# Kernel tuning notes

Hardware: AMD Instinct MI355X
Metric: run time of the kernel (lower is better)

## Reference

```python
import jax, jax.numpy as jnp
import numpy as np

B, T, V, C, K = 64, 128, 25, 128, 128
R = max(K // 4, 1)


def _ln(x, w, b, eps=1e-5):
    mu = jnp.mean(x, axis=-1, keepdims=True)
    var = jnp.mean((x - mu) ** 2, axis=-1, keepdims=True)
    return (x - mu) * jax.lax.rsqrt(var + eps) * w + b


def setup_inputs() -> dict:
    key = jax.random.key(0)
    ks = jax.random.split(key, 24)
    def w(i, shape, scale=0.05):
        return jax.random.normal(ks[i], shape, dtype=jnp.float32) * scale
    return {
        "x": jax.random.normal(ks[0], (B, T, V, C), dtype=jnp.float32),
        "A": jnp.broadcast_to(jnp.eye(V, dtype=jnp.float32), (K, V, V)) + 0.0,
        "lam": jnp.float32(0.1),
        "phi_w": w(1, (C, K)), "phi_b": w(2, (K,)),
        "theta_w": w(3, (C, K)), "theta_b": w(4, (K,)),
        "kappa_w": w(5, (K, K)), "kappa_b": w(6, (K,)),
        "xi_w": w(7, (C, K)), "xi_b": w(8, (K,)),
        "q_w": w(9, (K, K)), "q_b": w(10, (K,)),
        "k_w": w(11, (K, K)), "k_b": w(12, (K,)),
        "ca1_w": w(13, (K, R)), "ca1_b": w(14, (R,)),
        "ln1_w": jnp.ones((R,), jnp.float32), "ln1_b": jnp.zeros((R,), jnp.float32),
        "ca2_w": w(15, (R, K)), "ca2_b": w(16, (K,)),
        "ln2_w": jnp.ones((K,), jnp.float32), "ln2_b": jnp.zeros((K,), jnp.float32),
    }


def reference(x, A, lam, phi_w, phi_b, theta_w, theta_b, kappa_w, kappa_b,
              xi_w, xi_b, q_w, q_b, k_w, k_b, ca1_w, ca1_b, ln1_w, ln1_b,
              ca2_w, ca2_b, ln2_w, ln2_b):
    Bn, Tn, Vn, Cn = x.shape
    # dynamic adjacency from temporal-mean node features
    phi_x = (x @ phi_w + phi_b).mean(axis=1)      # [B,V,K]
    theta_x = (x @ theta_w + theta_b).mean(axis=1)  # [B,V,K]
    F_ij = jnp.tanh(phi_x[:, :, None, :] - theta_x[:, None, :, :])  # [B,V,V,K]
    A_hat = jnp.transpose(F_ij @ kappa_w + kappa_b, (0, 3, 1, 2))   # [B,K,V,V]
    A_tilde = A[None] + lam * A_hat                                 # [B,K,V,V]
    H = x @ xi_w + xi_b                                             # [B,T,V,K]
    # per-channel graph conv (avoids materializing [B*T*K,V,V])
    Z_gcn = jnp.einsum('bkuv,btvk->btuk', A_tilde, H)               # [B,T,V,K]
    # attention-modulated adjacency
    XQp = jnp.swapaxes((Z_gcn @ q_w + q_b).mean(axis=1), 1, 2)      # [B,K,V]
    XKp = jnp.swapaxes((Z_gcn @ k_w + k_b).mean(axis=1), 1, 2)      # [B,K,V]
    scale = float(np.sqrt(Tn))
    A_att = jax.nn.softmax(XQp[:, :, :, None] * XKp[:, :, None, :] / scale, axis=-1)  # [B,K,V,V]
    Z_A = jnp.einsum('btvk,bkuv->btuk', H, A_att)                   # [B,T,V,K]
    # channel attention gate
    ca = Z_A.mean(axis=(1, 2))                                      # [B,K]
    c1 = jax.nn.gelu(_ln(ca @ ca1_w + ca1_b, ln1_w, ln1_b), approximate=False)  # [B,R]
    gate = jax.nn.sigmoid(c1 @ ca2_w + ca2_b)                       # [B,K]
    A_c = A_tilde * gate[:, :, None, None]                          # [B,K,V,V]
    Z_G = jnp.einsum('bkuv,btvk->btuk', A_c, H)                     # [B,T,V,K]
    return _ln(Z_G, ln2_w, ln2_b)
```

## Files before the change

### kernel.cpp

```cpp
#include <hip/hip_runtime.h>
#include <hip/hip_bf16.h>
#include <math.h>

#define BB 64
#define TT 128
#define VV 25
#define CC 128
#define KK 128
#define RR 32
#define TG 4

typedef __attribute__((ext_vector_type(8))) short bf16x8;
typedef __attribute__((ext_vector_type(4))) float f32x4;

static __device__ __forceinline__ short f2bf(float f) {
    union { float f; unsigned u; } a; a.f = f;
    unsigned r = a.u + 0x7fffu + ((a.u >> 16) & 1u);
    return (short)(r >> 16);
}
static __device__ __forceinline__ float bf2f(short s) {
    union { unsigned u; float f; } a; a.u = ((unsigned)(unsigned short)s) << 16;
    return a.f;
}

#define WS_XBAR 0
#define WS_PHIX 204800
#define WS_THX  409600
#define WS_HBAR 614400
#define WS_XQ   819200
#define WS_XK   1024000
#define WS_CA   1228800
#define WS_GATE 1236992
#define WS_AT   1245184
#define WS_BT   6365184

__global__ __launch_bounds__(256) void kA(const float* __restrict__ x, float* __restrict__ xbar) {
    int row = blockIdx.x;
    int b = row / VV, v = row % VV;
    int tq = threadIdx.x >> 5, cq = threadIdx.x & 31;
    const float4* x4 = (const float4*)x;
    size_t base = ((size_t)b * TT * VV + v) * 32 + cq;
    float sx = 0.f, sy = 0.f, sz = 0.f, sw = 0.f;
    #pragma unroll 4
    for (int i = 0; i < 16; ++i) {
        float4 a = x4[base + (size_t)(tq * 16 + i) * VV * 32];
        sx += a.x; sy += a.y; sz += a.z; sw += a.w;
    }
    __shared__ float4 red[8][32];
    red[tq][cq] = (float4){sx, sy, sz, sw};
    __syncthreads();
    if (tq == 0) {
        float4 o = red[0][cq];
        #pragma unroll
        for (int j = 1; j < 8; ++j) {
            float4 a = red[j][cq];
            o.x += a.x; o.y += a.y; o.z += a.z; o.w += a.w;
        }
        o.x *= (1.f/TT); o.y *= (1.f/TT); o.z *= (1.f/TT); o.w *= (1.f/TT);
        ((float4*)xbar)[(size_t)row * 32 + cq] = o;
    }
}

__global__ __launch_bounds__(256) void kBT(const float* __restrict__ xw, short* __restrict__ BT) {
    for (int i = threadIdx.x + blockIdx.x * 256; i < KK * CC; i += 256 * 64) {
        int n = i >> 7, c = i & 127;
        BT[i] = f2bf(xw[c * KK + n]);
    }
}

__global__ __launch_bounds__(128) void kB1(const float* __restrict__ xbar,
        const float* __restrict__ pw, const float* __restrict__ pb,
        const float* __restrict__ tw, const float* __restrict__ tb,
        const float* __restrict__ xw, const float* __restrict__ xbias,
        float* __restrict__ phix, float* __restrict__ thx, float* __restrict__ hbar) {
    int bv = blockIdx.x;
    int k = threadIdx.x;
    __shared__ float xv[CC];
    xv[k] = xbar[(size_t)bv * CC + k];
    __syncthreads();
    float sp = pb[k], st = tb[k], sh = xbias[k];
    #pragma unroll 4
    for (int c = 0; c < CC; ++c) {
        float xc = xv[c];
        sp = fmaf(xc, pw[c*KK + k], sp);
        st = fmaf(xc, tw[c*KK + k], st);
        sh = fmaf(xc, xw[c*KK + k], sh);
    }
    phix[(size_t)bv*KK + k] = sp;
    thx [(size_t)bv*KK + k] = st;
    hbar[(size_t)bv*KK + k] = sh;
}

__global__ __launch_bounds__(128) void kB2(const float* __restrict__ phix, const float* __restrict__ thx,
        const float* __restrict__ kw, const float* __restrict__ kb,
        const float* __restrict__ A, const float* __restrict__ lam,
        short* __restrict__ At16) {
    int bi = blockIdx.x;
    int b = bi / VV, i = bi % VV;
    int k = threadIdx.x;
    __shared__ float f[VV][132];
    float ph = phix[((size_t)b*VV + i)*KK + k];
    #pragma unroll 5
    for (int j = 0; j < VV; ++j)
        f[j][k] = tanhf(ph - thx[((size_t)b*VV + j)*KK + k]);
    __syncthreads();
    float s[VV];
    float bias = kb[k];
    #pragma unroll
    for (int j = 0; j < VV; ++j) s[j] = bias;
    #pragma unroll 2
    for (int c = 0; c < CC; c += 4) {
        float w0 = kw[(c+0)*KK + k];
        float w1 = kw[(c+1)*KK + k];
        float w2 = kw[(c+2)*KK + k];
        float w3 = kw[(c+3)*KK + k];
        #pragma unroll
        for (int j = 0; j < VV; ++j) {
            float4 fv = *(const float4*)&f[j][c];
            float t = fmaf(fv.x, w0, fmaf(fv.y, w1, fmaf(fv.z, w2, fv.w * w3)));
            s[j] += t;
        }
    }
    float l = lam[0];
    #pragma unroll 5
    for (int j = 0; j < VV; ++j)
        At16[(((size_t)b*VV + i)*VV + j)*KK + k] = f2bf(A[((size_t)k*VV + i)*VV + j] + l * s[j]);
}

__global__ __launch_bounds__(128) void kB34(const short* __restrict__ At16, const float* __restrict__ hbar,
        const float* __restrict__ qw, const float* __restrict__ qb,
        const float* __restrict__ kw, const float* __restrict__ kb,
        float* __restrict__ XQ, float* __restrict__ XK) {
    int bu = blockIdx.x;
    int b = bu / VV;
    int k = threadIdx.x;
    __shared__ float zb[132];
    const short* at = At16 + ((size_t)bu * VV) * KK + k;
    const float* hb = hbar + (size_t)b * VV * KK + k;
    float s = 0.f;
    #pragma unroll
    for (int v = 0; v < VV; ++v) s = fmaf(bf2f(at[v*KK]), hb[v*KK], s);
    zb[k] = s;
    __syncthreads();
    float q = qb[k], kk2 = kb[k];
    #pragma unroll 2
    for (int c = 0; c < CC; c += 4) {
        float4 zv = *(const float4*)&zb[c];
        float q0 = qw[(c+0)*KK + k], q1 = qw[(c+1)*KK + k];
        float q2 = qw[(c+2)*KK + k], q3 = qw[(c+3)*KK + k];
        float k0 = kw[(c+0)*KK + k], k1 = kw[(c+1)*KK + k];
        float k2 = kw[(c+2)*KK + k], k3 = kw[(c+3)*KK + k];
        q   = fmaf(zv.x, q0, fmaf(zv.y, q1, fmaf(zv.z, q2, fmaf(zv.w, q3, q))));
        kk2 = fmaf(zv.x, k0, fmaf(zv.y, k1, fmaf(zv.z, k2, fmaf(zv.w, k3, kk2))));
    }
    XQ[(size_t)bu*KK + k] = q;
    XK[(size_t)bu*KK + k] = kk2;
}

__global__ __launch_bounds__(64) void kB5(const float* __restrict__ XQ, const float* __restrict__ XK,
        const float* __restrict__ hbar, float* __restrict__ ca) {
    int b = blockIdx.x >> 7;
    int k = blockIdx.x & 127;
    int tid = threadIdx.x;
    __shared__ float qv[VV], kv[VV], hv[VV], m[VV], dinv[VV];
    if (tid < VV) {
        qv[tid] = XQ[((size_t)b*VV + tid)*KK + k];
        kv[tid] = XK[((size_t)b*VV + tid)*KK + k];
        hv[tid] = hbar[((size_t)b*VV + tid)*KK + k];
    }
    __syncthreads();
    const float invs = 0.08838834764831845f;
    if (tid < VV) {
        float q = qv[tid];
        float mx = -1e30f;
        #pragma unroll
        for (int v = 0; v < VV; ++v) mx = fmaxf(mx, q * kv[v] * invs);
        float d = 0.f;
        #pragma unroll
        for (int v = 0; v < VV; ++v) d += expf(q * kv[v] * invs - mx);
        m[tid] = mx; dinv[tid] = 1.f / d;
    }
    __syncthreads();
    float contrib = 0.f;
    if (tid < VV) {
        float kkv = kv[tid];
        float s = 0.f;
        #pragma unroll
        for (int u = 0; u < VV; ++u) s += expf(qv[u] * kkv * invs - m[u]) * dinv[u];
        contrib = s * (1.f / VV) * hv[tid];
    }
    #pragma unroll
    for (int off = 32; off > 0; off >>= 1) contrib += __shfl_down(contrib, off);
    if (tid == 0) ca[(size_t)b*KK + k] = contrib;
}

__global__ __launch_bounds__(128) void kB6(const float* __restrict__ ca,
        const float* __restrict__ w1, const float* __restrict__ b1,
        const float* __restrict__ lw, const float* __restrict__ lb,
        const float* __restrict__ w2, const float* __restrict__ b2,
        float* __restrict__ gate) {
    int b = blockIdx.x;
    int tid = threadIdx.x;
    __shared__ float cas[KK], t1[RR], c1[RR];
    cas[tid] = ca[(size_t)b*KK + tid];
    __syncthreads();
    if (tid < RR) {
        float s = b1[tid];
        for (int c = 0; c < KK; ++c) s = fmaf(cas[c], w1[c*RR + tid], s);
        t1[tid] = s;
    }
    __syncthreads();
    if (tid < RR) {
        float mu = 0.f;
        #pragma unroll
        for (int j = 0; j < RR; ++j) mu += t1[j];
        mu *= (1.f / RR);
        float var = 0.f;
        #pragma unroll
        for (int j = 0; j < RR; ++j) { float d = t1[j] - mu; var = fmaf(d, d, var); }
        var *= (1.f / RR);
        float xn = (t1[tid] - mu) * rsqrtf(var + 1e-5f) * lw[tid] + lb[tid];
        c1[tid] = 0.5f * xn * (1.f + erff(xn * 0.70710678118654752f));
    }
    __syncthreads();
    float g = b2[tid];
    #pragma unroll
    for (int r = 0; r < RR; ++r) g = fmaf(c1[r], w2[r*KK + tid], g);
    gate[(size_t)b*KK + tid] = 1.f / (1.f + expf(-g));
}

#define HP 132
__global__ __launch_bounds__(256, 3) void kF(const float* __restrict__ x,
        const short* __restrict__ BT, const float* __restrict__ xbias,
        const short* __restrict__ At16, const float* __restrict__ gate,
        const float* __restrict__ lw, const float* __restrict__ lb,
        float* __restrict__ out) {
    int b  = blockIdx.x >> 5;
    int tg = blockIdx.x & 31;
    int t0 = tg * TG;
    int tid = threadIdx.x;
    int wave = tid >> 6, lane = tid & 63;
    int l15 = lane & 15, quad = lane >> 4;

    __shared__ short Hs[TG * 32 * HP];
    __shared__ float ms[TG * 32], rs[TG * 32];

    {
        const float* xw_base = x + ((size_t)(b * TT + t0 + wave) * VV) * CC;
        f32x4 acc[2][8];
        #pragma unroll
        for (int rt = 0; rt < 2; ++rt)
            #pragma unroll
            for (int ct = 0; ct < 8; ++ct)
                acc[rt][ct] = (f32x4){0.f, 0.f, 0.f, 0.f};

        int va0 = l15;
        int va1 = 16 + l15;
        if (va1 > VV - 1) va1 = VV - 1;

        #pragma unroll
        for (int s = 0; s < 4; ++s) {
            bf16x8 afr[2];
            #pragma unroll
            for (int rt = 0; rt < 2; ++rt) {
                const float* ap = xw_base + (size_t)(rt ? va1 : va0) * CC + s*32 + quad*8;
                float4 a0 = *(const float4*)ap;
                float4 a1 = *(const float4*)(ap + 4);
                union { bf16x8 v; short h[8]; } u;
                u.h[0] = f2bf(a0.x); u.h[1] = f2bf(a0.y); u.h[2] = f2bf(a0.z); u.h[3] = f2bf(a0.w);
                u.h[4] = f2bf(a1.x); u.h[5] = f2bf(a1.y); u.h[6] = f2bf(a1.z); u.h[7] = f2bf(a1.w);
                afr[rt] = u.v;
            }
            #pragma unroll
            for (int ct = 0; ct < 8; ++ct) {
                bf16x8 bfr = *(const bf16x8*)(BT + (ct*16 + l15) * CC + s*32 + quad*8);
                acc[0][ct] = __builtin_amdgcn_mfma_f32_16x16x32_bf16(afr[0], bfr, acc[0][ct], 0, 0, 0);
                acc[1][ct] = __builtin_amdgcn_mfma_f32_16x16x32_bf16(afr[1], bfr, acc[1][ct], 0, 0, 0);
            }
        }
        #pragma unroll
        for (int ct = 0; ct < 8; ++ct) {
            float bias = xbias[ct*16 + l15];
            #pragma unroll
            for (int rt = 0; rt < 2; ++rt) {
                int vbase = rt*16 + quad*4;
                #pragma unroll
                for (int i = 0; i < 4; ++i)
                    Hs[(wave*32 + vbase + i) * HP + ct*16 + l15] = f2bf(acc[rt][ct][i] + bias);
            }
        }
    }
    __syncthreads();

    int k = tid & 127, g = tid >> 7;
    int tt0 = 2*g, tt1 = 2*g + 1;

    float h0[VV], h1[VV];
    #pragma unroll
    for (int v = 0; v < VV; ++v) {
        h0[v] = bf2f(Hs[(tt0*32 + v) * HP + k]);
        h1[v] = bf2f(Hs[(tt1*32 + v) * HP + k]);
    }

    float gv = gate[(size_t)b * KK + k];
    const short* atb = At16 + ((size_t)b * VV * VV) * KK + k;
    short z0s[VV], z1s[VV];
    #pragma unroll 1
    for (int u = 0; u < VV; ++u) {
        float z0 = 0.f, z1 = 0.f;
        #pragma unroll
        for (int v = 0; v < VV; ++v) {
            float a = bf2f(atb[(u * VV + v) * KK]);
            z0 = fmaf(a, h0[v], z0);
            z1 = fmaf(a, h1[v], z1);
        }
        z0s[u] = f2bf(z0 * gv);
        z1s[u] = f2bf(z1 * gv);
    }
    __syncthreads();

    #pragma unroll
    for (int u = 0; u < VV; ++u) {
        Hs[(tt0*32 + u) * HP + k] = z0s[u];
        Hs[(tt1*32 + u) * HP + k] = z1s[u];
    }
    __syncthreads();

    if (tid < 128) {
        int u = tid & 31;
        if (u < VV) {
            const short4* zr = (const short4*)(Hs + tid * HP);
            float s = 0.f, s2 = 0.f;
            #pragma unroll 8
            for (int i = 0; i < KK/4; ++i) {
                short4 q = zr[i];
                float a = bf2f(q.x), bq = bf2f(q.y), c = bf2f(q.z), d = bf2f(q.w);
                s += a + bq + c + d;
                s2 = fmaf(a, a, fmaf(bq, bq, fmaf(c, c, fmaf(d, d, s2))));
            }
            float mu = s * (1.f / KK);
            float var = s2 * (1.f / KK) - mu * mu;
            ms[tid] = mu;
            rs[tid] = rsqrtf(var + 1e-5f);
        }
    }
    __syncthreads();

    float w2 = lw[k], b2v = lb[k];
    #pragma unroll 1
    for (int tt = tt0; tt <= tt1; ++tt) {
        float* ob = out + (((size_t)(b * TT + t0 + tt)) * VV) * KK + k;
        #pragma unroll
        for (int u = 0; u < VV; ++u) {
            float val = (bf2f(Hs[(tt*32 + u) * HP + k]) - ms[tt*32 + u]) * rs[tt*32 + u] * w2 + b2v;
            ob[(size_t)u * KK] = val;
        }
    }
}

extern "C" void kernel_launch(void* const* d_in, const int* in_sizes, int n_in,
                              void* d_out, int out_size, void* d_ws, size_t ws_size,
                              hipStream_t stream) {
    const float* x      = (const float*)d_in[0];
    const float* A      = (const float*)d_in[1];
    const float* lam    = (const float*)d_in[2];
    const float* phi_w  = (const float*)d_in[3];
    const float* phi_b  = (const float*)d_in[4];
    const float* th_w   = (const float*)d_in[5];
    const float* th_b   = (const float*)d_in[6];
    const float* ka_w   = (const float*)d_in[7];
    const float* ka_b   = (const float*)d_in[8];
    const float* xi_w   = (const float*)d_in[9];
    const float* xi_b   = (const float*)d_in[10];
    const float* q_w    = (const float*)d_in[11];
    const float* q_b    = (const float*)d_in[12];
    const float* k_w    = (const float*)d_in[13];
    const float* k_b    = (const float*)d_in[14];
    const float* ca1_w  = (const float*)d_in[15];
    const float* ca1_b  = (const float*)d_in[16];
    const float* ln1_w  = (const float*)d_in[17];
    const float* ln1_b  = (const float*)d_in[18];
    const float* ca2_w  = (const float*)d_in[19];
    const float* ca2_b  = (const float*)d_in[20];
    const float* ln2_w  = (const float*)d_in[21];
    const float* ln2_b  = (const float*)d_in[22];
    float* out = (float*)d_out;
    float* ws  = (float*)d_ws;
    short* At16 = (short*)(ws + WS_AT);
    short* BT  = (short*)(ws + WS_BT);

    kBT <<<64, 256, 0, stream>>>(xi_w, BT);
    kA  <<<BB*VV, 256, 0, stream>>>(x, ws + WS_XBAR);
    kB1 <<<BB*VV, 128, 0, stream>>>(ws + WS_XBAR, phi_w, phi_b, th_w, th_b, xi_w, xi_b,
                                    ws + WS_PHIX, ws + WS_THX, ws + WS_HBAR);
    kB2 <<<BB*VV, 128, 0, stream>>>(ws + WS_PHIX, ws + WS_THX, ka_w, ka_b, A, lam, At16);
    kB34<<<BB*VV, 128, 0, stream>>>(At16, ws + WS_HBAR, q_w, q_b, k_w, k_b,
                                    ws + WS_XQ, ws + WS_XK);
    kB5 <<<BB*KK, 64, 0, stream>>>(ws + WS_XQ, ws + WS_XK, ws + WS_HBAR, ws + WS_CA);
    kB6 <<<BB, 128, 0, stream>>>(ws + WS_CA, ca1_w, ca1_b, ln1_w, ln1_b, ca2_w, ca2_b, ws + WS_GATE);
    kF  <<<BB*(TT/TG), 256, 0, stream>>>(x, BT, xi_b, At16, ws + WS_GATE, ln2_w, ln2_b, out);
}
```

Baseline: 471.9 us.

## Pack adjacency per (u,k) as contiguous bf16 vectors and prefetch in kF

Changes the adjacency buffer layout so each (b,u,k) stores its 25 v-values padded to 32 contiguous bf16, letting kB34 and kF load them with four 128-bit loads instead of 25 strided short loads. kF software-prefetches the next row, writes conv results directly to shared memory (dropping register staging), and uses nontemporal output stores. The padded layout enlarges the workspace region, which may overlap following buffers if offsets were not adjusted.

```diff
diff --git a/kernel.cpp b/kernel.cpp
--- a/kernel.cpp
+++ b/kernel.cpp
@@ -94,7 +94,7 @@
 __global__ __launch_bounds__(128) void kB2(const float* __restrict__ phix, const float* __restrict__ thx,
         const float* __restrict__ kw, const float* __restrict__ kb,
         const float* __restrict__ A, const float* __restrict__ lam,
-        short* __restrict__ At16) {
+        short* __restrict__ Atv) {
     int bi = blockIdx.x;
     int b = bi / VV, i = bi % VV;
     int k = threadIdx.x;
@@ -122,12 +122,25 @@
         }
     }
     float l = lam[0];
-    #pragma unroll 5
+    float vals[32];
+    #pragma unroll
     for (int j = 0; j < VV; ++j)
-        At16[(((size_t)b*VV + i)*VV + j)*KK + k] = f2bf(A[((size_t)k*VV + i)*VV + j] + l * s[j]);
-}
-
-__global__ __launch_bounds__(128) void kB34(const short* __restrict__ At16, const float* __restrict__ hbar,
+        vals[j] = A[((size_t)k*VV + i)*VV + j] + l * s[j];
+    #pragma unroll
+    for (int j = VV; j < 32; ++j) vals[j] = 0.f;
+    unsigned dw[16];
+    #pragma unroll
+    for (int m = 0; m < 16; ++m)
+        dw[m] = (unsigned)(unsigned short)f2bf(vals[2*m])
+              | ((unsigned)(unsigned short)f2bf(vals[2*m+1]) << 16);
+    uint4* dst = (uint4*)(Atv + ((size_t)bi * KK + k) * 32);
+    dst[0] = make_uint4(dw[0],  dw[1],  dw[2],  dw[3]);
+    dst[1] = make_uint4(dw[4],  dw[5],  dw[6],  dw[7]);
+    dst[2] = make_uint4(dw[8],  dw[9],  dw[10], dw[11]);
+    dst[3] = make_uint4(dw[12], dw[13], dw[14], dw[15]);
+}
+
+__global__ __launch_bounds__(128) void kB34(const short* __restrict__ Atv, const float* __restrict__ hbar,
         const float* __restrict__ qw, const float* __restrict__ qb,
         const float* __restrict__ kw, const float* __restrict__ kb,
         float* __restrict__ XQ, float* __restrict__ XK) {
@@ -135,11 +148,19 @@
     int b = bu / VV;
     int k = threadIdx.x;
     __shared__ float zb[132];
-    const short* at = At16 + ((size_t)bu * VV) * KK + k;
     const float* hb = hbar + (size_t)b * VV * KK + k;
+    const uint4* av = (const uint4*)(Atv + ((size_t)bu * KK + k) * 32);
+    uint4 a0 = av[0], a1 = av[1], a2 = av[2], a3 = av[3];
     float s = 0.f;
-    #pragma unroll
-    for (int v = 0; v < VV; ++v) s = fmaf(bf2f(at[v*KK]), hb[v*KK], s);
+#define KB34S(dd, v0) { \
+    float lo_ = __uint_as_float((unsigned)(dd) << 16); \
+    float hi_ = __uint_as_float((unsigned)(dd) & 0xffff0000u); \
+    s = fmaf(lo_, hb[(v0)*KK], s); s = fmaf(hi_, hb[((v0)+1)*KK], s); }
+    KB34S(a0.x, 0)  KB34S(a0.y, 2)  KB34S(a0.z, 4)  KB34S(a0.w, 6)
+    KB34S(a1.x, 8)  KB34S(a1.y, 10) KB34S(a1.z, 12) KB34S(a1.w, 14)
+    KB34S(a2.x, 16) KB34S(a2.y, 18) KB34S(a2.z, 20) KB34S(a2.w, 22)
+    { float lo_ = __uint_as_float((unsigned)a3.x << 16); s = fmaf(lo_, hb[24*KK], s); }
+#undef KB34S
     zb[k] = s;
     __syncthreads();
     float q = qb[k], kk2 = kb[k];
@@ -232,7 +253,7 @@
 #define HP 132
 __global__ __launch_bounds__(256, 3) void kF(const float* __restrict__ x,
         const short* __restrict__ BT, const float* __restrict__ xbias,
-        const short* __restrict__ At16, const float* __restrict__ gate,
+        const short* __restrict__ Atv, const float* __restrict__ gate,
         const float* __restrict__ lw, const float* __restrict__ lb,
         float* __restrict__ out) {
     int b  = blockIdx.x >> 5;
@@ -290,10 +311,14 @@
             }
         }
     }
-    __syncthreads();
 
     int k = tid & 127, g = tid >> 7;
     int tt0 = 2*g, tt1 = 2*g + 1;
+    float gv = gate[(size_t)b * KK + k];
+    const uint4* ap = (const uint4*)(Atv + ((size_t)(b * VV) * KK + k) * 32);
+    uint4 c0 = ap[0], c1 = ap[1], c2 = ap[2], c3 = ap[3];
+
+    __syncthreads();
 
     float h0[VV], h1[VV];
     #pragma unroll
@@ -301,29 +326,29 @@
         h0[v] = bf2f(Hs[(tt0*32 + v) * HP + k]);
         h1[v] = bf2f(Hs[(tt1*32 + v) * HP + k]);
     }
-
-    float gv = gate[(size_t)b * KK + k];
-    const short* atb = At16 + ((size_t)b * VV * VV) * KK + k;
-    short z0s[VV], z1s[VV];
+    __syncthreads();
+
+#define CONVSTEP(dd, v0) { \
+    float lo_ = __uint_as_float((unsigned)(dd) << 16); \
+    float hi_ = __uint_as_float((unsigned)(dd) & 0xffff0000u); \
+    za0 = fmaf(lo_, h0[v0], za0); zb0 = fmaf(hi_, h0[(v0)+1], zb0); \
+    za1 = fmaf(lo_, h1[v0], za1); zb1 = fmaf(hi_, h1[(v0)+1], zb1); }
+
     #pragma unroll 1
     for (int u = 0; u < VV; ++u) {
-        float z0 = 0.f, z1 = 0.f;
-        #pragma unroll
-        for (int v = 0; v < VV; ++v) {
-            float a = bf2f(atb[(u * VV + v) * KK]);
-            z0 = fmaf(a, h0[v], z0);
-            z1 = fmaf(a, h1[v], z1);
-        }
-        z0s[u] = f2bf(z0 * gv);
-        z1s[u] = f2bf(z1 * gv);
-    }
-    __syncthreads();
-
-    #pragma unroll
-    for (int u = 0; u < VV; ++u) {
-        Hs[(tt0*32 + u) * HP + k] = z0s[u];
-        Hs[(tt1*32 + u) * HP + k] = z1s[u];
-    }
+        const uint4* np = ap + ((u < VV-1) ? (KK*4) : 0);
+        uint4 n0 = np[0], n1 = np[1], n2 = np[2], n3 = np[3];
+        float za0 = 0.f, zb0 = 0.f, za1 = 0.f, zb1 = 0.f;
+        CONVSTEP(c0.x, 0)  CONVSTEP(c0.y, 2)  CONVSTEP(c0.z, 4)  CONVSTEP(c0.w, 6)
+        CONVSTEP(c1.x, 8)  CONVSTEP(c1.y, 10) CONVSTEP(c1.z, 12) CONVSTEP(c1.w, 14)
+        CONVSTEP(c2.x, 16) CONVSTEP(c2.y, 18) CONVSTEP(c2.z, 20) CONVSTEP(c2.w, 22)
+        { float lo_ = __uint_as_float((unsigned)c3.x << 16);
+          za0 = fmaf(lo_, h0[24], za0); za1 = fmaf(lo_, h1[24], za1); }
+        Hs[(tt0*32 + u) * HP + k] = f2bf((za0 + zb0) * gv);
+        Hs[(tt1*32 + u) * HP + k] = f2bf((za1 + zb1) * gv);
+        ap = np; c0 = n0; c1 = n1; c2 = n2; c3 = n3;
+    }
+#undef CONVSTEP
     __syncthreads();
 
     if (tid < 128) {
@@ -353,7 +378,7 @@
         #pragma unroll
         for (int u = 0; u < VV; ++u) {
             float val = (bf2f(Hs[(tt*32 + u) * HP + k]) - ms[tt*32 + u]) * rs[tt*32 + u] * w2 + b2v;
-            ob[(size_t)u * KK] = val;
+            __builtin_nontemporal_store(val, ob + (size_t)u * KK);
         }
     }
 }
@@ -386,17 +411,17 @@
     const float* ln2_b  = (const float*)d_in[22];
     float* out = (float*)d_out;
     float* ws  = (float*)d_ws;
-    short* At16 = (short*)(ws + WS_AT);
+    short* Atv = (short*)(ws + WS_AT);
     short* BT  = (short*)(ws + WS_BT);
 
     kBT <<<64, 256, 0, stream>>>(xi_w, BT);
     kA  <<<BB*VV, 256, 0, stream>>>(x, ws + WS_XBAR);
     kB1 <<<BB*VV, 128, 0, stream>>>(ws + WS_XBAR, phi_w, phi_b, th_w, th_b, xi_w, xi_b,
                                     ws + WS_PHIX, ws + WS_THX, ws + WS_HBAR);
-    kB2 <<<BB*VV, 128, 0, stream>>>(ws + WS_PHIX, ws + WS_THX, ka_w, ka_b, A, lam, At16);
-    kB34<<<BB*VV, 128, 0, stream>>>(At16, ws + WS_HBAR, q_w, q_b, k_w, k_b,
+    kB2 <<<BB*VV, 128, 0, stream>>>(ws + WS_PHIX, ws + WS_THX, ka_w, ka_b, A, lam, Atv);
+    kB34<<<BB*VV, 128, 0, stream>>>(Atv, ws + WS_HBAR, q_w, q_b, k_w, k_b,
                                     ws + WS_XQ, ws + WS_XK);
     kB5 <<<BB*KK, 64, 0, stream>>>(ws + WS_XQ, ws + WS_XK, ws + WS_HBAR, ws + WS_CA);
     kB6 <<<BB, 128, 0, stream>>>(ws + WS_CA, ca1_w, ca1_b, ln1_w, ln1_b, ca2_w, ca2_b, ws + WS_GATE);
-    kF  <<<BB*(TT/TG), 256, 0, stream>>>(x, BT, xi_b, At16, ws + WS_GATE, ln2_w, ln2_b, out);
-}
+    kF  <<<BB*(TT/TG), 256, 0, stream>>>(x, BT, xi_b, Atv, ws + WS_GATE, ln2_w, ln2_b, out);
+}
```

Measured after the change: 412.7 us. -12.6%, faster.
